# Kernel optimization log

Hardware: AMD Instinct MI355X
Metric: run time of the kernel (lower is better)

Reference implementation:

```python
import jax, jax.numpy as jnp
import numpy as np

B, L, D = 4, 2048, 256
DI, DS, DCONV, DTR, K = 512, 16, 4, 16, 3  # d_inner, d_state, mamba conv, dt_rank, outer conv kernel
PAD = 1 * (K - 1)  # dilation*(kernel_size-1)
ALPHA = 0.5


def setup_inputs() -> dict:
    key = jax.random.key(0)
    ks = jax.random.split(key, 14)
    s = lambda k, shape, scale: jax.random.normal(k, shape, dtype=jnp.float32) * scale
    inp = {
        "x": s(ks[0], (B, L, D), 1.0),
        "ln_w": jnp.ones((D,), jnp.float32),
        "ln_b": jnp.zeros((D,), jnp.float32),
        "conv_w": s(ks[1], (D, D, K), 0.05),          # outer Conv1d weight (out,in,k)
        "conv_b": s(ks[2], (D,), 0.02),
        "in_proj_w": s(ks[3], (2 * DI, D), 0.05),      # Mamba in_proj (no bias)
        "conv1d_w": s(ks[4], (DI, 1, DCONV), 0.3),     # depthwise causal conv
        "conv1d_b": s(ks[5], (DI,), 0.02),
        "x_proj_w": s(ks[6], (DTR + 2 * DS, DI), 0.05),
        "dt_proj_w": s(ks[7], (DI, DTR), 0.1),
        "dt_proj_b": s(ks[8], (DI,), 0.1),
        "A_log": jnp.log(jnp.broadcast_to(jnp.arange(1, DS + 1, dtype=jnp.float32), (DI, DS))),
        "D_param": jnp.ones((DI,), jnp.float32),
        "out_proj_w": s(ks[9], (D, DI), 0.05),
    }
    return inp


def _layernorm(h, w, b):
    mu = jnp.mean(h, axis=-1, keepdims=True)
    var = jnp.mean(jnp.square(h - mu), axis=-1, keepdims=True)
    return (h - mu) * jax.lax.rsqrt(var + 1e-5) * w + b


def _causal_conv(h_ncl, w, pad, groups):
    # h_ncl: (B, C, L); left-pad only -> output length L (matches pad-then-slice in torch)
    return jax.lax.conv_general_dilated(
        h_ncl, w, window_strides=(1,), padding=[(pad, 0)],
        dimension_numbers=("NCH", "OIH", "NCH"), feature_group_count=groups)


def _mamba(h, in_proj_w, conv1d_w, conv1d_b, x_proj_w, dt_proj_w, dt_proj_b, A_log, D_param, out_proj_w):
    xz = jnp.einsum("bld,ed->ble", h, in_proj_w)          # (B,L,2*DI)
    xin, z = jnp.split(xz, 2, axis=-1)
    xc = _causal_conv(xin.transpose(0, 2, 1), conv1d_w, DCONV - 1, DI)
    xc = jax.nn.silu(xc + conv1d_b[None, :, None]).transpose(0, 2, 1)   # (B,L,DI)
    x_dbl = jnp.einsum("bld,ed->ble", xc, x_proj_w)
    dt, Bm, Cm = jnp.split(x_dbl, [DTR, DTR + DS], axis=-1)
    delta = jax.nn.softplus(jnp.einsum("blr,dr->bld", dt, dt_proj_w) + dt_proj_b)  # (B,L,DI)
    A = -jnp.exp(A_log)                                     # (DI,DS)
    dA = jnp.exp(delta[..., None] * A)                      # (B,L,DI,DS)
    dBx = delta[..., None] * Bm[:, :, None, :] * xc[..., None]

    def step(hst, t):
        dA_t, dBx_t, C_t = t
        hst = dA_t * hst + dBx_t                            # (B,DI,DS)
        y = jnp.einsum("bds,bs->bd", hst, C_t)
        return hst, y

    h0 = jnp.zeros((h.shape[0], DI, DS), h.dtype)
    _, ys = jax.lax.scan(step, h0, (dA.transpose(1, 0, 2, 3), dBx.transpose(1, 0, 2, 3), Cm.transpose(1, 0, 2)))
    y = ys.transpose(1, 0, 2) + xc * D_param                # (B,L,DI)
    y = y * jax.nn.silu(z)
    return jnp.einsum("ble,de->bld", y, out_proj_w)


def reference(x, ln_w, ln_b, conv_w, conv_b, in_proj_w, conv1d_w, conv1d_b,
              x_proj_w, dt_proj_w, dt_proj_b, A_log, D_param, out_proj_w):
    h = _layernorm(x, ln_w, ln_b)
    # conv branch: pad left, conv, GELU (exact erf, as torch nn.GELU)
    hc = _causal_conv(h.transpose(0, 2, 1), conv_w, PAD, 1) + conv_b[None, :, None]
    h_conv = jax.nn.gelu(hc, approximate=False).transpose(0, 2, 1)
    h_mamba = _mamba(h, in_proj_w, conv1d_w, conv1d_b, x_proj_w, dt_proj_w,
                     dt_proj_b, A_log, D_param, out_proj_w)
    h_out = ALPHA * h_mamba + (1.0 - ALPHA) * h_conv
    return x + h_out
```

## Files before the change

kernel.cpp:

```cpp
#include <hip/hip_runtime.h>
#include <math.h>

#define BBATCH 4
#define LSEQ   2048
#define DMODEL 256
#define DINNER 512
#define DSTATE 16
#define DTRANK 16
#define MROWS  (BBATCH * LSEQ)
#define NCHUNK 64
#define LCHUNK (LSEQ / NCHUNK)

typedef unsigned short u16;
typedef __attribute__((ext_vector_type(8))) short bf16x8;
typedef __attribute__((ext_vector_type(4))) float f32x4;

#define OFF_HBF    ((size_t)0)
#define OFF_HCONV  ((size_t)1048576)
#define OFF_XIN    ((size_t)3145728)
#define OFF_Z      ((size_t)7340032)
#define OFF_XC     ((size_t)11534336)
#define OFF_DELTA  ((size_t)15728640)
#define OFF_XDBL   ((size_t)19922944)
#define OFF_YBF    ((size_t)20316160)
#define OFF_AAGG   ((size_t)22413312)
#define OFF_BAGG   ((size_t)24510464)
#define OFF_HINIT  OFF_AAGG
#define OFF_WTINBF ((size_t)26607616)
#define OFF_WTCVBF ((size_t)26738688)
#define OFF_WTOUTBF ((size_t)26836992)
#define OFF_WTX    ((size_t)26902528)
#define OFF_WTDT   ((size_t)26927104)

__device__ __forceinline__ float silu_f(float v) {
  return v / (1.0f + __expf(-v));
}
__device__ __forceinline__ u16 f2bf(float f) {
  unsigned u = __float_as_uint(f);
  return (u16)((u + 0x7FFFu + ((u >> 16) & 1u)) >> 16);
}

__global__ __launch_bounds__(256) void k_repack(
    const float* __restrict__ inw, const float* __restrict__ convw,
    const float* __restrict__ xw, const float* __restrict__ dtw,
    const float* __restrict__ ow, float* __restrict__ ws) {
  int idx = blockIdx.x * 256 + threadIdx.x;
  u16* win  = (u16*)(ws + OFF_WTINBF);
  u16* wcv  = (u16*)(ws + OFF_WTCVBF);
  u16* wout = (u16*)(ws + OFF_WTOUTBF);
  float* wx  = ws + OFF_WTX;
  float* wdt = ws + OFF_WTDT;
  if (idx < 262144) {
    win[idx] = f2bf(inw[idx]);
    return;
  }
  int i2 = idx - 262144;
  if (i2 < 196608) {
    int o = i2 / 768, r = i2 - o * 768;
    int kk = r >> 8, i = r & 255;
    wcv[i2] = f2bf(convw[(o * 256 + i) * 3 + kk]);
    return;
  }
  int i3 = i2 - 196608;
  if (i3 < 131072) {
    wout[i3] = f2bf(ow[i3]);
    return;
  }
  int i4 = i3 - 131072;
  if (i4 < 24576) {
    int k = i4 / 48, n = i4 - k * 48;
    wx[i4] = xw[n * 512 + k];
    return;
  }
  int i5 = i4 - 24576;
  if (i5 < 8192) {
    int r = i5 >> 9, n = i5 & 511;
    wdt[i5] = dtw[n * 16 + r];
  }
}

__global__ __launch_bounds__(256) void k_layernorm(
    const float* __restrict__ x, const float* __restrict__ w,
    const float* __restrict__ b, u16* __restrict__ hb) {
  int wave = threadIdx.x >> 6;
  int lane = threadIdx.x & 63;
  int row  = blockIdx.x * 4 + wave;
  const float4* xr = reinterpret_cast<const float4*>(x + (size_t)row * 256);
  float4 v = xr[lane];
  float s  = v.x + v.y + v.z + v.w;
  float sq = v.x*v.x + v.y*v.y + v.z*v.z + v.w*v.w;
  #pragma unroll
  for (int o = 32; o >= 1; o >>= 1) { s += __shfl_xor(s, o); sq += __shfl_xor(sq, o); }
  float mu  = s * (1.0f / 256.0f);
  float var = sq * (1.0f / 256.0f) - mu * mu;
  float rs  = rsqrtf(var + 1e-5f);
  float4 wv = reinterpret_cast<const float4*>(w)[lane];
  float4 bv = reinterpret_cast<const float4*>(b)[lane];
  ushort4 o4;
  o4.x = f2bf((v.x - mu) * rs * wv.x + bv.x);
  o4.y = f2bf((v.y - mu) * rs * wv.y + bv.y);
  o4.z = f2bf((v.z - mu) * rs * wv.z + bv.z);
  o4.w = f2bf((v.w - mu) * rs * wv.w + bv.w);
  reinterpret_cast<ushort4*>(hb + (size_t)row * 256)[lane] = o4;
}


__global__ __launch_bounds__(256) void k_bgemm_inproj(
    const u16* __restrict__ Abf, const u16* __restrict__ Bbf,
    float* __restrict__ xin, float* __restrict__ z) {
  __shared__ __align__(16) u16 As[64 * 72];
  __shared__ __align__(16) u16 Bs[64 * 72];
  int tid = threadIdx.x;
  int m0 = blockIdx.x * 64, n0 = blockIdx.y * 64;
  int lane = tid & 63, wid = tid >> 6;
  int wr = (wid >> 1) * 32, wc = (wid & 1) * 32;
  int l15 = lane & 15, lk = (lane >> 4) * 8;
  int r0 = tid >> 3, kc = (tid & 7) * 8;
  f32x4 acc[2][2] = {};
  for (int k0 = 0; k0 < 256; k0 += 64) {
    *(bf16x8*)&As[r0 * 72 + kc] =
        *(const bf16x8*)&Abf[(size_t)(m0 + r0) * 256 + k0 + kc];
    *(bf16x8*)&As[(r0 + 32) * 72 + kc] =
        *(const bf16x8*)&Abf[(size_t)(m0 + r0 + 32) * 256 + k0 + kc];
    *(bf16x8*)&Bs[r0 * 72 + kc] =
        *(const bf16x8*)&Bbf[(size_t)(n0 + r0) * 256 + k0 + kc];
    *(bf16x8*)&Bs[(r0 + 32) * 72 + kc] =
        *(const bf16x8*)&Bbf[(size_t)(n0 + r0 + 32) * 256 + k0 + kc];
    __syncthreads();
    #pragma unroll
    for (int kk = 0; kk < 64; kk += 32) {
      bf16x8 a0 = *(const bf16x8*)&As[(wr + l15) * 72 + kk + lk];
      bf16x8 a1 = *(const bf16x8*)&As[(wr + 16 + l15) * 72 + kk + lk];
      bf16x8 b0 = *(const bf16x8*)&Bs[(wc + l15) * 72 + kk + lk];
      bf16x8 b1 = *(const bf16x8*)&Bs[(wc + 16 + l15) * 72 + kk + lk];
      acc[0][0] = __builtin_amdgcn_mfma_f32_16x16x32_bf16(a0, b0, acc[0][0], 0, 0, 0);
      acc[0][1] = __builtin_amdgcn_mfma_f32_16x16x32_bf16(a0, b1, acc[0][1], 0, 0, 0);
      acc[1][0] = __builtin_amdgcn_mfma_f32_16x16x32_bf16(a1, b0, acc[1][0], 0, 0, 0);
      acc[1][1] = __builtin_amdgcn_mfma_f32_16x16x32_bf16(a1, b1, acc[1][1], 0, 0, 0);
    }
    __syncthreads();
  }
  float* dst = (n0 < 512) ? xin : z;
  int nb = (n0 < 512) ? n0 : n0 - 512;
  int rowb = m0 + wr + (lane >> 4) * 4;
  #pragma unroll
  for (int mi = 0; mi < 2; ++mi)
    #pragma unroll
    for (int ni = 0; ni < 2; ++ni) {
      int gc = nb + wc + ni * 16 + l15;
      #pragma unroll
      for (int r = 0; r < 4; ++r)
        dst[(size_t)(rowb + mi * 16 + r) * 512 + gc] = acc[mi][ni][r];
    }
}

__global__ __launch_bounds__(256) void k_bgemm_conv(
    const u16* __restrict__ hbf, const u16* __restrict__ Bbf,
    const float* __restrict__ cb, float* __restrict__ hconv) {
  __shared__ __align__(16) u16 As[64 * 72];
  __shared__ __align__(16) u16 Bs[64 * 72];
  int tid = threadIdx.x;
  int m0 = blockIdx.x * 64, n0 = blockIdx.y * 64;
  int bidx = m0 >> 11, t0 = m0 & 2047;
  int lane = tid & 63, wid = tid >> 6;
  int wr = (wid >> 1) * 32, wc = (wid & 1) * 32;
  int l15 = lane & 15, lk = (lane >> 4) * 8;
  int r0 = tid >> 3, kc = (tid & 7) * 8;
  f32x4 acc[2][2] = {};
  for (int k0 = 0; k0 < 768; k0 += 64) {
    int kkc = k0 >> 8;
    int i0  = (k0 & 255) + kc;
    int t1  = t0 + r0 - 2 + kkc;
    bf16x8 av0 = {0, 0, 0, 0, 0, 0, 0, 0};
    if (t1 >= 0)
      av0 = *(const bf16x8*)&hbf[(size_t)((bidx << 11) + t1) * 256 + i0];
    bf16x8 av1 =
        *(const bf16x8*)&hbf[(size_t)((bidx << 11) + t1 + 32) * 256 + i0];
    *(bf16x8*)&As[r0 * 72 + kc] = av0;
    *(bf16x8*)&As[(r0 + 32) * 72 + kc] = av1;
    *(bf16x8*)&Bs[r0 * 72 + kc] =
        *(const bf16x8*)&Bbf[(size_t)(n0 + r0) * 768 + k0 + kc];
    *(bf16x8*)&Bs[(r0 + 32) * 72 + kc] =
        *(const bf16x8*)&Bbf[(size_t)(n0 + r0 + 32) * 768 + k0 + kc];
    __syncthreads();
    #pragma unroll
    for (int kk = 0; kk < 64; kk += 32) {
      bf16x8 a0 = *(const bf16x8*)&As[(wr + l15) * 72 + kk + lk];
      bf16x8 a1 = *(const bf16x8*)&As[(wr + 16 + l15) * 72 + kk + lk];
      bf16x8 b0 = *(const bf16x8*)&Bs[(wc + l15) * 72 + kk + lk];
      bf16x8 b1 = *(const bf16x8*)&Bs[(wc + 16 + l15) * 72 + kk + lk];
      acc[0][0] = __builtin_amdgcn_mfma_f32_16x16x32_bf16(a0, b0, acc[0][0], 0, 0, 0);
      acc[0][1] = __builtin_amdgcn_mfma_f32_16x16x32_bf16(a0, b1, acc[0][1], 0, 0, 0);
      acc[1][0] = __builtin_amdgcn_mfma_f32_16x16x32_bf16(a1, b0, acc[1][0], 0, 0, 0);
      acc[1][1] = __builtin_amdgcn_mfma_f32_16x16x32_bf16(a1, b1, acc[1][1], 0, 0, 0);
    }
    __syncthreads();
  }
  int rowb = m0 + wr + (lane >> 4) * 4;
  #pragma unroll
  for (int mi = 0; mi < 2; ++mi)
    #pragma unroll
    for (int ni = 0; ni < 2; ++ni) {
      int gc = n0 + wc + ni * 16 + l15;
      float bias = cb[gc];
      #pragma unroll
      for (int r = 0; r < 4; ++r) {
        float v = acc[mi][ni][r] + bias;
        float g = 0.5f * v * (1.0f + erff(v * 0.70710678118654752440f));
        hconv[(size_t)(rowb + mi * 16 + r) * 256 + gc] = g;
      }
    }
}

__global__ __launch_bounds__(256) void k_bgemm_outproj(
    const u16* __restrict__ Abf, const u16* __restrict__ Bbf,
    const float* __restrict__ x, const float* __restrict__ hconv,
    float* __restrict__ out) {
  __shared__ __align__(16) u16 As[64 * 72];
  __shared__ __align__(16) u16 Bs[64 * 72];
  int tid = threadIdx.x;
  int m0 = blockIdx.x * 64, n0 = blockIdx.y * 64;
  int lane = tid & 63, wid = tid >> 6;
  int wr = (wid >> 1) * 32, wc = (wid & 1) * 32;
  int l15 = lane & 15, lk = (lane >> 4) * 8;
  int r0 = tid >> 3, kc = (tid & 7) * 8;
  f32x4 acc[2][2] = {};
  for (int k0 = 0; k0 < 512; k0 += 64) {
    *(bf16x8*)&As[r0 * 72 + kc] =
        *(const bf16x8*)&Abf[(size_t)(m0 + r0) * 512 + k0 + kc];
    *(bf16x8*)&As[(r0 + 32) * 72 + kc] =
        *(const bf16x8*)&Abf[(size_t)(m0 + r0 + 32) * 512 + k0 + kc];
    *(bf16x8*)&Bs[r0 * 72 + kc] =
        *(const bf16x8*)&Bbf[(size_t)(n0 + r0) * 512 + k0 + kc];
    *(bf16x8*)&Bs[(r0 + 32) * 72 + kc] =
        *(const bf16x8*)&Bbf[(size_t)(n0 + r0 + 32) * 512 + k0 + kc];
    __syncthreads();
    #pragma unroll
    for (int kk = 0; kk < 64; kk += 32) {
      bf16x8 a0 = *(const bf16x8*)&As[(wr + l15) * 72 + kk + lk];
      bf16x8 a1 = *(const bf16x8*)&As[(wr + 16 + l15) * 72 + kk + lk];
      bf16x8 b0 = *(const bf16x8*)&Bs[(wc + l15) * 72 + kk + lk];
      bf16x8 b1 = *(const bf16x8*)&Bs[(wc + 16 + l15) * 72 + kk + lk];
      acc[0][0] = __builtin_amdgcn_mfma_f32_16x16x32_bf16(a0, b0, acc[0][0], 0, 0, 0);
      acc[0][1] = __builtin_amdgcn_mfma_f32_16x16x32_bf16(a0, b1, acc[0][1], 0, 0, 0);
      acc[1][0] = __builtin_amdgcn_mfma_f32_16x16x32_bf16(a1, b0, acc[1][0], 0, 0, 0);
      acc[1][1] = __builtin_amdgcn_mfma_f32_16x16x32_bf16(a1, b1, acc[1][1], 0, 0, 0);
    }
    __syncthreads();
  }
  int rowb = m0 + wr + (lane >> 4) * 4;
  #pragma unroll
  for (int mi = 0; mi < 2; ++mi)
    #pragma unroll
    for (int ni = 0; ni < 2; ++ni) {
      int gc = n0 + wc + ni * 16 + l15;
      #pragma unroll
      for (int r = 0; r < 4; ++r) {
        size_t off = (size_t)(rowb + mi * 16 + r) * 256 + gc;
        out[off] = x[off] + 0.5f * acc[mi][ni][r] + 0.5f * hconv[off];
      }
    }
}

__global__ __launch_bounds__(256) void k_gemm_xproj(
    const float* __restrict__ A, const float* __restrict__ Bt,
    float* __restrict__ C) {
  __shared__ float As[16][68];
  __shared__ float Bs[16][68];
  int tid = threadIdx.x;
  int m0 = blockIdx.x * 64;
  int ar = tid >> 2, ac = (tid & 3) * 4;
  int br = tid >> 4, bc = (tid & 15) * 4;
  int tx = tid & 15, ty = tid >> 4;
  float acc[4][4] = {};
  for (int k0 = 0; k0 < 512; k0 += 16) {
    float4 av = *reinterpret_cast<const float4*>(A + (size_t)(m0 + ar) * 512 + k0 + ac);
    As[ac + 0][ar] = av.x; As[ac + 1][ar] = av.y;
    As[ac + 2][ar] = av.z; As[ac + 3][ar] = av.w;
    float4 bv = make_float4(0.f, 0.f, 0.f, 0.f);
    if (bc < 48)
      bv = *reinterpret_cast<const float4*>(Bt + (size_t)(k0 + br) * 48 + bc);
    *reinterpret_cast<float4*>(&Bs[br][bc]) = bv;
    __syncthreads();
    #pragma unroll
    for (int kt = 0; kt < 16; ++kt) {
      float4 a = *reinterpret_cast<const float4*>(&As[kt][ty * 4]);
      float4 b = *reinterpret_cast<const float4*>(&Bs[kt][tx * 4]);
      acc[0][0]+=a.x*b.x; acc[0][1]+=a.x*b.y; acc[0][2]+=a.x*b.z; acc[0][3]+=a.x*b.w;
      acc[1][0]+=a.y*b.x; acc[1][1]+=a.y*b.y; acc[1][2]+=a.y*b.z; acc[1][3]+=a.y*b.w;
      acc[2][0]+=a.z*b.x; acc[2][1]+=a.z*b.y; acc[2][2]+=a.z*b.z; acc[2][3]+=a.z*b.w;
      acc[3][0]+=a.w*b.x; acc[3][1]+=a.w*b.y; acc[3][2]+=a.w*b.z; acc[3][3]+=a.w*b.w;
    }
    __syncthreads();
  }
  if (tx < 12) {
    #pragma unroll
    for (int i = 0; i < 4; ++i) {
      float4 cv = make_float4(acc[i][0], acc[i][1], acc[i][2], acc[i][3]);
      *reinterpret_cast<float4*>(C + (size_t)(m0 + ty * 4 + i) * 48 + tx * 4) = cv;
    }
  }
}

__global__ __launch_bounds__(256) void k_dwconv(
    const float* __restrict__ xin, const float* __restrict__ cw,
    const float* __restrict__ cb, float* __restrict__ xc) {
  int idx = blockIdx.x * 256 + threadIdx.x;
  int di = idx & 511;
  int m  = idx >> 9;
  int t  = m & 2047;
  float w0 = cw[di * 4 + 0], w1 = cw[di * 4 + 1];
  float w2 = cw[di * 4 + 2], w3 = cw[di * 4 + 3];
  const float* base = xin + (size_t)m * 512 + di;
  float acc = cb[di] + w3 * base[0];
  if (t >= 1) acc += w2 * base[-512];
  if (t >= 2) acc += w1 * base[-1024];
  if (t >= 3) acc += w0 * base[-1536];
  xc[(size_t)m * 512 + di] = silu_f(acc);
}

__global__ __launch_bounds__(256) void k_dtproj(
    const float* __restrict__ xdbl, const float* __restrict__ Wdt,
    const float* __restrict__ db, float* __restrict__ delta) {
  int m = blockIdx.x;
  __shared__ float dts[16];
  if (threadIdx.x < 16) dts[threadIdx.x] = xdbl[(size_t)m * 48 + threadIdx.x];
  __syncthreads();
  for (int di = threadIdx.x; di < 512; di += 256) {
    float acc = db[di];
    #pragma unroll
    for (int r = 0; r < 16; ++r) acc += dts[r] * Wdt[r * 512 + di];
    delta[(size_t)m * 512 + di] = (acc > 20.0f) ? acc : log1pf(__expf(acc));
  }
}

__global__ __launch_bounds__(256) void k_scan1(
    const float* __restrict__ delta, const float* __restrict__ xdbl,
    const float* __restrict__ xc, const float* __restrict__ Alog,
    float* __restrict__ Aagg, float* __restrict__ Bagg) {
  int di = ((blockIdx.x & 1) << 8) | threadIdx.x;
  int c  = (blockIdx.x >> 1) & 63;
  int b  = blockIdx.x >> 7;
  float nA[16];
  #pragma unroll
  for (int q = 0; q < 4; ++q) {
    float4 v = *reinterpret_cast<const float4*>(Alog + (size_t)di * 16 + q * 4);
    nA[q*4+0] = -__expf(v.x); nA[q*4+1] = -__expf(v.y);
    nA[q*4+2] = -__expf(v.z); nA[q*4+3] = -__expf(v.w);
  }
  float ap[16], bacc[16];
  #pragma unroll
  for (int s = 0; s < 16; ++s) { ap[s] = 1.0f; bacc[s] = 0.0f; }
  int row0 = b * 2048 + c * LCHUNK;
  const float* dp = delta + (size_t)row0 * 512 + di;
  const float* xp = xc    + (size_t)row0 * 512 + di;
  const float* Bp = xdbl  + (size_t)row0 * 48 + 16;
  #pragma unroll 2
  for (int t = 0; t < LCHUNK; ++t) {
    float dv = dp[t * 512];
    float u  = dv * xp[t * 512];
    #pragma unroll
    for (int s = 0; s < 16; ++s) {
      float e = __expf(dv * nA[s]);
      ap[s]   *= e;
      bacc[s]  = e * bacc[s] + u * Bp[t * 48 + s];
    }
  }
  size_t base = ((size_t)((b * 64 + c) * 16)) * 512 + di;
  #pragma unroll
  for (int s = 0; s < 16; ++s) {
    Aagg[base + (size_t)s * 512] = ap[s];
    Bagg[base + (size_t)s * 512] = bacc[s];
  }
}

__global__ __launch_bounds__(256) void k_scan2(
    const float* __restrict__ Aagg, const float* __restrict__ Bagg,
    float* __restrict__ Hinit) {
  int g  = blockIdx.x * 256 + threadIdx.x;
  int di = g & 511, s = (g >> 9) & 15, b = g >> 13;
  float h = 0.0f;
  for (int c = 0; c < NCHUNK; ++c) {
    size_t idx = ((size_t)((b * 64 + c) * 16 + s)) * 512 + di;
    float a = Aagg[idx], bb = Bagg[idx];
    Hinit[idx] = h;
    h = a * h + bb;
  }
}

__global__ __launch_bounds__(256) void k_scan3(
    const float* __restrict__ delta, const float* __restrict__ xdbl,
    const float* __restrict__ xc, const float* __restrict__ z,
    const float* __restrict__ Alog, const float* __restrict__ Dp,
    const float* __restrict__ Hinit, u16* __restrict__ y) {
  int di = ((blockIdx.x & 1) << 8) | threadIdx.x;
  int c  = (blockIdx.x >> 1) & 63;
  int b  = blockIdx.x >> 7;
  float nA[16];
  #pragma unroll
  for (int q = 0; q < 4; ++q) {
    float4 v = *reinterpret_cast<const float4*>(Alog + (size_t)di * 16 + q * 4);
    nA[q*4+0] = -__expf(v.x); nA[q*4+1] = -__expf(v.y);
    nA[q*4+2] = -__expf(v.z); nA[q*4+3] = -__expf(v.w);
  }
  float h[16];
  size_t hb = ((size_t)((b * 64 + c) * 16)) * 512 + di;
  #pragma unroll
  for (int s = 0; s < 16; ++s) h[s] = Hinit[hb + (size_t)s * 512];
  float Dv = Dp[di];
  int row0 = b * 2048 + c * LCHUNK;
  const float* dp = delta + (size_t)row0 * 512 + di;
  const float* xp = xc    + (size_t)row0 * 512 + di;
  const float* zp = z     + (size_t)row0 * 512 + di;
  const float* Bp = xdbl  + (size_t)row0 * 48 + 16;
  const float* Cp = xdbl  + (size_t)row0 * 48 + 32;
  u16* yp         = y     + (size_t)row0 * 512 + di;
  #pragma unroll 2
  for (int t = 0; t < LCHUNK; ++t) {
    float dv  = dp[t * 512];
    float xcv = xp[t * 512];
    float u   = dv * xcv;
    float yv  = 0.0f;
    #pragma unroll
    for (int s = 0; s < 16; ++s) {
      float e = __expf(dv * nA[s]);
      h[s] = e * h[s] + u * Bp[t * 48 + s];
      yv  += h[s] * Cp[t * 48 + s];
    }
    yv += xcv * Dv;
    float zv = zp[t * 512];
    yp[t * 512] = f2bf(yv * silu_f(zv));
  }
}

extern "C" void kernel_launch(void* const* d_in, const int* in_sizes, int n_in,
                              void* d_out, int out_size, void* d_ws, size_t ws_size,
                              hipStream_t stream) {
  const float* x     = (const float*)d_in[0];
  const float* lnw   = (const float*)d_in[1];
  const float* lnb   = (const float*)d_in[2];
  const float* convw = (const float*)d_in[3];
  const float* convb = (const float*)d_in[4];
  const float* inw   = (const float*)d_in[5];
  const float* c1w   = (const float*)d_in[6];
  const float* c1b   = (const float*)d_in[7];
  const float* xw    = (const float*)d_in[8];
  const float* dtw   = (const float*)d_in[9];
  const float* dtb   = (const float*)d_in[10];
  const float* alog  = (const float*)d_in[11];
  const float* Dp    = (const float*)d_in[12];
  const float* ow    = (const float*)d_in[13];
  float* ws  = (float*)d_ws;
  float* out = (float*)d_out;

  u16* hbf    = (u16*)(ws + OFF_HBF);
  float* hconv = ws + OFF_HCONV;
  float* xin   = ws + OFF_XIN;
  float* zb    = ws + OFF_Z;
  float* xc    = ws + OFF_XC;
  float* delta = ws + OFF_DELTA;
  float* xdbl  = ws + OFF_XDBL;
  u16* ybf    = (u16*)(ws + OFF_YBF);
  float* Aagg  = ws + OFF_AAGG;
  float* Bagg  = ws + OFF_BAGG;
  float* Hinit = ws + OFF_HINIT;
  u16* winbf  = (u16*)(ws + OFF_WTINBF);
  u16* wcvbf  = (u16*)(ws + OFF_WTCVBF);
  u16* woutbf = (u16*)(ws + OFF_WTOUTBF);
  float* Wtx   = ws + OFF_WTX;
  float* Wtdt  = ws + OFF_WTDT;

  k_repack<<<2432, 256, 0, stream>>>(inw, convw, xw, dtw, ow, ws);
  k_layernorm<<<2048, 256, 0, stream>>>(x, lnw, lnb, hbf);
  k_bgemm_conv<<<dim3(128, 4), 256, 0, stream>>>(hbf, wcvbf, convb, hconv);
  k_bgemm_inproj<<<dim3(128, 16), 256, 0, stream>>>(hbf, winbf, xin, zb);
  k_dwconv<<<16384, 256, 0, stream>>>(xin, c1w, c1b, xc);
  k_gemm_xproj<<<dim3(128, 1), 256, 0, stream>>>(xc, Wtx, xdbl);
  k_dtproj<<<8192, 256, 0, stream>>>(xdbl, Wtdt, dtb, delta);
  k_scan1<<<512, 256, 0, stream>>>(delta, xdbl, xc, alog, Aagg, Bagg);
  k_scan2<<<128, 256, 0, stream>>>(Aagg, Bagg, Hinit);
  k_scan3<<<512, 256, 0, stream>>>(delta, xdbl, xc, zb, alog, Dp, Hinit, ybf);
  k_bgemm_outproj<<<dim3(128, 4), 256, 0, stream>>>(ybf, woutbf, x, hconv, out);
}
```

Measured before the change: 254.0 us.

## Store in_proj outputs as bf16, widen its N tile, fuse dt_proj into x_proj

The in_proj GEMM now uses 64x128 tiles and writes xin and z as bf16 instead of fp32, which halves the traffic for those intermediates and for their readers in dwconv and scan3. The dt_proj GEMV plus softplus is folded into the x_proj kernel through a shared-memory staging of the dt columns, which removes one launch and a reread of xdbl. In exchange, xin and z lose precision through bf16 rounding, and the fused kernel has only 128 blocks, each running a serial 64-row delta loop that could limit parallelism.

```diff
diff --git a/kernel.cpp b/kernel.cpp
--- a/kernel.cpp
+++ b/kernel.cpp
@@ -39,6 +39,9 @@
   unsigned u = __float_as_uint(f);
   return (u16)((u + 0x7FFFu + ((u >> 16) & 1u)) >> 16);
 }
+__device__ __forceinline__ float bf2f(u16 v) {
+  return __uint_as_float(((unsigned)v) << 16);
+}
 
 __global__ __launch_bounds__(256) void k_repack(
     const float* __restrict__ inw, const float* __restrict__ convw,
@@ -107,50 +110,50 @@
 
 __global__ __launch_bounds__(256) void k_bgemm_inproj(
     const u16* __restrict__ Abf, const u16* __restrict__ Bbf,
-    float* __restrict__ xin, float* __restrict__ z) {
+    u16* __restrict__ xin, u16* __restrict__ z) {
   __shared__ __align__(16) u16 As[64 * 72];
-  __shared__ __align__(16) u16 Bs[64 * 72];
+  __shared__ __align__(16) u16 Bs[128 * 72];
   int tid = threadIdx.x;
-  int m0 = blockIdx.x * 64, n0 = blockIdx.y * 64;
+  int m0 = blockIdx.x * 64, n0 = blockIdx.y * 128;
   int lane = tid & 63, wid = tid >> 6;
-  int wr = (wid >> 1) * 32, wc = (wid & 1) * 32;
+  int wc = wid * 32;
   int l15 = lane & 15, lk = (lane >> 4) * 8;
   int r0 = tid >> 3, kc = (tid & 7) * 8;
-  f32x4 acc[2][2] = {};
+  f32x4 acc[4][2] = {};
   for (int k0 = 0; k0 < 256; k0 += 64) {
     *(bf16x8*)&As[r0 * 72 + kc] =
         *(const bf16x8*)&Abf[(size_t)(m0 + r0) * 256 + k0 + kc];
     *(bf16x8*)&As[(r0 + 32) * 72 + kc] =
         *(const bf16x8*)&Abf[(size_t)(m0 + r0 + 32) * 256 + k0 + kc];
-    *(bf16x8*)&Bs[r0 * 72 + kc] =
-        *(const bf16x8*)&Bbf[(size_t)(n0 + r0) * 256 + k0 + kc];
-    *(bf16x8*)&Bs[(r0 + 32) * 72 + kc] =
-        *(const bf16x8*)&Bbf[(size_t)(n0 + r0 + 32) * 256 + k0 + kc];
+    #pragma unroll
+    for (int rr = 0; rr < 4; ++rr)
+      *(bf16x8*)&Bs[(r0 + rr * 32) * 72 + kc] =
+          *(const bf16x8*)&Bbf[(size_t)(n0 + r0 + rr * 32) * 256 + k0 + kc];
     __syncthreads();
     #pragma unroll
     for (int kk = 0; kk < 64; kk += 32) {
-      bf16x8 a0 = *(const bf16x8*)&As[(wr + l15) * 72 + kk + lk];
-      bf16x8 a1 = *(const bf16x8*)&As[(wr + 16 + l15) * 72 + kk + lk];
       bf16x8 b0 = *(const bf16x8*)&Bs[(wc + l15) * 72 + kk + lk];
       bf16x8 b1 = *(const bf16x8*)&Bs[(wc + 16 + l15) * 72 + kk + lk];
-      acc[0][0] = __builtin_amdgcn_mfma_f32_16x16x32_bf16(a0, b0, acc[0][0], 0, 0, 0);
-      acc[0][1] = __builtin_amdgcn_mfma_f32_16x16x32_bf16(a0, b1, acc[0][1], 0, 0, 0);
-      acc[1][0] = __builtin_amdgcn_mfma_f32_16x16x32_bf16(a1, b0, acc[1][0], 0, 0, 0);
-      acc[1][1] = __builtin_amdgcn_mfma_f32_16x16x32_bf16(a1, b1, acc[1][1], 0, 0, 0);
-    }
-    __syncthreads();
-  }
-  float* dst = (n0 < 512) ? xin : z;
-  int nb = (n0 < 512) ? n0 : n0 - 512;
-  int rowb = m0 + wr + (lane >> 4) * 4;
-  #pragma unroll
-  for (int mi = 0; mi < 2; ++mi)
+      #pragma unroll
+      for (int q = 0; q < 4; ++q) {
+        bf16x8 a = *(const bf16x8*)&As[(q * 16 + l15) * 72 + kk + lk];
+        acc[q][0] = __builtin_amdgcn_mfma_f32_16x16x32_bf16(a, b0, acc[q][0], 0, 0, 0);
+        acc[q][1] = __builtin_amdgcn_mfma_f32_16x16x32_bf16(a, b1, acc[q][1], 0, 0, 0);
+      }
+    }
+    __syncthreads();
+  }
+  u16* dst = (blockIdx.y < 4) ? xin : z;
+  int nb = n0 & 511;
+  int rsub = (lane >> 4) * 4;
+  #pragma unroll
+  for (int q = 0; q < 4; ++q)
     #pragma unroll
     for (int ni = 0; ni < 2; ++ni) {
       int gc = nb + wc + ni * 16 + l15;
       #pragma unroll
       for (int r = 0; r < 4; ++r)
-        dst[(size_t)(rowb + mi * 16 + r) * 512 + gc] = acc[mi][ni][r];
+        dst[(size_t)(m0 + q * 16 + rsub + r) * 512 + gc] = f2bf(acc[q][ni][r]);
     }
 }
 
@@ -262,11 +265,13 @@
     }
 }
 
-__global__ __launch_bounds__(256) void k_gemm_xproj(
+__global__ __launch_bounds__(256) void k_xdt(
     const float* __restrict__ A, const float* __restrict__ Bt,
-    float* __restrict__ C) {
+    const float* __restrict__ Wdt, const float* __restrict__ db,
+    float* __restrict__ xdbl, float* __restrict__ delta) {
   __shared__ float As[16][68];
   __shared__ float Bs[16][68];
+  __shared__ float dts[64][17];
   int tid = threadIdx.x;
   int m0 = blockIdx.x * 64;
   int ar = tid >> 2, ac = (tid & 3) * 4;
@@ -297,13 +302,40 @@
     #pragma unroll
     for (int i = 0; i < 4; ++i) {
       float4 cv = make_float4(acc[i][0], acc[i][1], acc[i][2], acc[i][3]);
-      *reinterpret_cast<float4*>(C + (size_t)(m0 + ty * 4 + i) * 48 + tx * 4) = cv;
-    }
+      *reinterpret_cast<float4*>(xdbl + (size_t)(m0 + ty * 4 + i) * 48 + tx * 4) = cv;
+    }
+  }
+  if (tx < 4) {
+    #pragma unroll
+    for (int i = 0; i < 4; ++i)
+      #pragma unroll
+      for (int j = 0; j < 4; ++j)
+        dts[ty * 4 + i][tx * 4 + j] = acc[i][j];
+  }
+  __syncthreads();
+  int di = tid;
+  float wv0[16], wv1[16];
+  #pragma unroll
+  for (int r = 0; r < 16; ++r) {
+    wv0[r] = Wdt[r * 512 + di];
+    wv1[r] = Wdt[r * 512 + di + 256];
+  }
+  float bb0 = db[di], bb1 = db[di + 256];
+  for (int m = 0; m < 64; ++m) {
+    float a0 = bb0, a1 = bb1;
+    #pragma unroll
+    for (int r = 0; r < 16; ++r) {
+      float d = dts[m][r];
+      a0 += d * wv0[r];
+      a1 += d * wv1[r];
+    }
+    delta[(size_t)(m0 + m) * 512 + di]       = (a0 > 20.0f) ? a0 : log1pf(__expf(a0));
+    delta[(size_t)(m0 + m) * 512 + di + 256] = (a1 > 20.0f) ? a1 : log1pf(__expf(a1));
   }
 }
 
 __global__ __launch_bounds__(256) void k_dwconv(
-    const float* __restrict__ xin, const float* __restrict__ cw,
+    const u16* __restrict__ xin, const float* __restrict__ cw,
     const float* __restrict__ cb, float* __restrict__ xc) {
   int idx = blockIdx.x * 256 + threadIdx.x;
   int di = idx & 511;
@@ -311,27 +343,12 @@
   int t  = m & 2047;
   float w0 = cw[di * 4 + 0], w1 = cw[di * 4 + 1];
   float w2 = cw[di * 4 + 2], w3 = cw[di * 4 + 3];
-  const float* base = xin + (size_t)m * 512 + di;
-  float acc = cb[di] + w3 * base[0];
-  if (t >= 1) acc += w2 * base[-512];
-  if (t >= 2) acc += w1 * base[-1024];
-  if (t >= 3) acc += w0 * base[-1536];
+  const u16* base = xin + (size_t)m * 512 + di;
+  float acc = cb[di] + w3 * bf2f(base[0]);
+  if (t >= 1) acc += w2 * bf2f(base[-512]);
+  if (t >= 2) acc += w1 * bf2f(base[-1024]);
+  if (t >= 3) acc += w0 * bf2f(base[-1536]);
   xc[(size_t)m * 512 + di] = silu_f(acc);
-}
-
-__global__ __launch_bounds__(256) void k_dtproj(
-    const float* __restrict__ xdbl, const float* __restrict__ Wdt,
-    const float* __restrict__ db, float* __restrict__ delta) {
-  int m = blockIdx.x;
-  __shared__ float dts[16];
-  if (threadIdx.x < 16) dts[threadIdx.x] = xdbl[(size_t)m * 48 + threadIdx.x];
-  __syncthreads();
-  for (int di = threadIdx.x; di < 512; di += 256) {
-    float acc = db[di];
-    #pragma unroll
-    for (int r = 0; r < 16; ++r) acc += dts[r] * Wdt[r * 512 + di];
-    delta[(size_t)m * 512 + di] = (acc > 20.0f) ? acc : log1pf(__expf(acc));
-  }
 }
 
 __global__ __launch_bounds__(256) void k_scan1(
@@ -390,7 +407,7 @@
 
 __global__ __launch_bounds__(256) void k_scan3(
     const float* __restrict__ delta, const float* __restrict__ xdbl,
-    const float* __restrict__ xc, const float* __restrict__ z,
+    const float* __restrict__ xc, const u16* __restrict__ z,
     const float* __restrict__ Alog, const float* __restrict__ Dp,
     const float* __restrict__ Hinit, u16* __restrict__ y) {
   int di = ((blockIdx.x & 1) << 8) | threadIdx.x;
@@ -411,7 +428,7 @@
   int row0 = b * 2048 + c * LCHUNK;
   const float* dp = delta + (size_t)row0 * 512 + di;
   const float* xp = xc    + (size_t)row0 * 512 + di;
-  const float* zp = z     + (size_t)row0 * 512 + di;
+  const u16*   zp = z     + (size_t)row0 * 512 + di;
   const float* Bp = xdbl  + (size_t)row0 * 48 + 16;
   const float* Cp = xdbl  + (size_t)row0 * 48 + 32;
   u16* yp         = y     + (size_t)row0 * 512 + di;
@@ -428,7 +445,7 @@
       yv  += h[s] * Cp[t * 48 + s];
     }
     yv += xcv * Dv;
-    float zv = zp[t * 512];
+    float zv = bf2f(zp[t * 512]);
     yp[t * 512] = f2bf(yv * silu_f(zv));
   }
 }
@@ -453,32 +470,31 @@
   float* ws  = (float*)d_ws;
   float* out = (float*)d_out;
 
-  u16* hbf    = (u16*)(ws + OFF_HBF);
+  u16* hbf     = (u16*)(ws + OFF_HBF);
   float* hconv = ws + OFF_HCONV;
-  float* xin   = ws + OFF_XIN;
-  float* zb    = ws + OFF_Z;
+  u16* xinbf   = (u16*)(ws + OFF_XIN);
+  u16* zbf     = (u16*)(ws + OFF_Z);
   float* xc    = ws + OFF_XC;
   float* delta = ws + OFF_DELTA;
   float* xdbl  = ws + OFF_XDBL;
-  u16* ybf    = (u16*)(ws + OFF_YBF);
+  u16* ybf     = (u16*)(ws + OFF_YBF);
   float* Aagg  = ws + OFF_AAGG;
   float* Bagg  = ws + OFF_BAGG;
   float* Hinit = ws + OFF_HINIT;
-  u16* winbf  = (u16*)(ws + OFF_WTINBF);
-  u16* wcvbf  = (u16*)(ws + OFF_WTCVBF);
-  u16* woutbf = (u16*)(ws + OFF_WTOUTBF);
+  u16* winbf   = (u16*)(ws + OFF_WTINBF);
+  u16* wcvbf   = (u16*)(ws + OFF_WTCVBF);
+  u16* woutbf  = (u16*)(ws + OFF_WTOUTBF);
   float* Wtx   = ws + OFF_WTX;
   float* Wtdt  = ws + OFF_WTDT;
 
   k_repack<<<2432, 256, 0, stream>>>(inw, convw, xw, dtw, ow, ws);
   k_layernorm<<<2048, 256, 0, stream>>>(x, lnw, lnb, hbf);
   k_bgemm_conv<<<dim3(128, 4), 256, 0, stream>>>(hbf, wcvbf, convb, hconv);
-  k_bgemm_inproj<<<dim3(128, 16), 256, 0, stream>>>(hbf, winbf, xin, zb);
-  k_dwconv<<<16384, 256, 0, stream>>>(xin, c1w, c1b, xc);
-  k_gemm_xproj<<<dim3(128, 1), 256, 0, stream>>>(xc, Wtx, xdbl);
-  k_dtproj<<<8192, 256, 0, stream>>>(xdbl, Wtdt, dtb, delta);
+  k_bgemm_inproj<<<dim3(128, 8), 256, 0, stream>>>(hbf, winbf, xinbf, zbf);
+  k_dwconv<<<16384, 256, 0, stream>>>(xinbf, c1w, c1b, xc);
+  k_xdt<<<128, 256, 0, stream>>>(xc, Wtx, Wtdt, dtb, xdbl, delta);
   k_scan1<<<512, 256, 0, stream>>>(delta, xdbl, xc, alog, Aagg, Bagg);
   k_scan2<<<128, 256, 0, stream>>>(Aagg, Bagg, Hinit);
-  k_scan3<<<512, 256, 0, stream>>>(delta, xdbl, xc, zb, alog, Dp, Hinit, ybf);
+  k_scan3<<<512, 256, 0, stream>>>(delta, xdbl, xc, zbf, alog, Dp, Hinit, ybf);
   k_bgemm_outproj<<<dim3(128, 4), 256, 0, stream>>>(ybf, woutbf, x, hconv, out);
 }
```

Result: slower. 282.0 us (+11.0%).
